# Kernel tuning notes

Measured on AMD Instinct MI355X. Metric: run time of the kernel, lower is better.

The kernel has to match this reference:

```python
import jax, jax.numpy as jnp
import numpy as np
import math

# dims
BSZ, L, D = 2, 4096, 1024
EXPAND, DS, NH, NG, DC, CS = 2, 128, 32, 1, 4, 64
DI = EXPAND * D            # 2048
HP = DI // NH              # 64 headdim
D_IN_PROJ = 2 * DI + 2 * NG * DS + NH  # 4384
CONV_DIM = DI + 2 * NG * DS            # 2304
EPS = 1e-5


def setup_inputs() -> dict:
    key = jax.random.key(0)
    ks = jax.random.split(key, 10)
    u = jax.random.normal(ks[0], (BSZ, L, D), dtype=jnp.float32)
    W_in = jax.random.normal(ks[1], (D, D_IN_PROJ), dtype=jnp.float32) / math.sqrt(D)
    conv_w = jax.random.normal(ks[2], (CONV_DIM, DC), dtype=jnp.float32) / math.sqrt(DC)
    conv_b = jnp.zeros((CONV_DIM,), dtype=jnp.float32)
    # dt init as in module: dt ~ logspace(1e-3, 0.1), dt_bias = inv softplus
    dt = jnp.exp(jax.random.uniform(ks[3], (NH,)) * (math.log(0.1) - math.log(0.001)) + math.log(0.001))
    dt = jnp.clip(dt, 1e-4, None)
    dt_bias = dt + jnp.log(-jnp.expm1(-dt))
    A_log = jnp.log(jax.random.uniform(ks[4], (NH,), minval=1.0, maxval=16.0))
    norm_w = jnp.ones((DI,), dtype=jnp.float32)
    norm_b = jnp.zeros((DI,), dtype=jnp.float32)
    W_out = jax.random.normal(ks[5], (DI, D), dtype=jnp.float32) / math.sqrt(DI)
    return {"u": u, "W_in": W_in, "conv_w": conv_w, "conv_b": conv_b,
            "dt_bias": dt_bias, "A_log": A_log, "norm_w": norm_w,
            "norm_b": norm_b, "W_out": W_out}


def _segsum(x):
    # x: (..., l) -> (..., l, l), out[i,j] = sum_{j<t<=i} x[t], -inf above diag
    cs = jnp.cumsum(x, axis=-1)
    d = cs[..., :, None] - cs[..., None, :]
    n = x.shape[-1]
    mask = jnp.tril(jnp.ones((n, n), dtype=bool))
    return jnp.where(mask, d, -jnp.inf)


def _ssd(x, A, Bm, Cm):
    # x: (b,l,h,p) already scaled by dt; A: (b,l,h) = a*dt; Bm,Cm: (b,l,h,n)
    b, l, h, p = x.shape
    nc = l // CS
    x = x.reshape(b, nc, CS, h, p)
    A = A.reshape(b, nc, CS, h).transpose(0, 3, 1, 2)          # (b,h,c,s)
    Bm = Bm.reshape(b, nc, CS, h, -1)
    Cm = Cm.reshape(b, nc, CS, h, -1)
    A_cum = jnp.cumsum(A, axis=-1)                              # (b,h,c,s)
    Lmat = jnp.exp(_segsum(A))                                  # (b,h,c,s,s)
    # intra-chunk (diagonal block) output
    Yd = jnp.einsum('bclhn,bcshn,bhcls,bcshp->bclhp', Cm, Bm, Lmat, x)
    # per-chunk final states
    decay_states = jnp.exp(A_cum[..., -1:] - A_cum)             # (b,h,c,s)
    states = jnp.einsum('bcshn,bhcs,bcshp->bchpn', Bm, decay_states, x)
    # inter-chunk recurrence (parallel via segsum over chunk decays)
    A_chunk = jnp.pad(A_cum[..., -1], ((0, 0), (0, 0), (1, 0)))  # (b,h,c+1)
    decay_chunk = jnp.exp(_segsum(A_chunk))                      # (b,h,c+1,c+1)
    states0 = jnp.concatenate([jnp.zeros_like(states[:, :1]), states], axis=1)
    new_states = jnp.einsum('bhzc,bchpn->bzhpn', decay_chunk, states0)
    states_in = new_states[:, :-1]                               # (b,c,h,p,n)
    state_decay = jnp.exp(A_cum)                                 # (b,h,c,s)
    Yoff = jnp.einsum('bcshn,bchpn,bhcs->bcshp', Cm, states_in, state_decay)
    return (Yd + Yoff).reshape(b, l, h, p)


def _causal_dwconv(x, w, b):
    # x: (B,L,C), depthwise causal conv, kernel w: (C,K), bias b: (C,)
    k = w.shape[1]
    xp = jnp.pad(x, ((0, 0), (k - 1, 0), (0, 0)))
    seqlen = x.shape[1]
    out = b
    for i in range(k):  # small fixed kernel loop (K=4)
        out = out + xp[:, i:i + seqlen, :] * w[:, i]
    return out


def reference(u, W_in, conv_w, conv_b, dt_bias, A_log, norm_w, norm_b, W_out):
    b, l, _ = u.shape
    zxbcdt = u @ W_in                                  # (b,l,2*DI+2*NG*DS+NH)
    z = zxbcdt[..., :DI]
    xBC = zxbcdt[..., DI:DI + CONV_DIM]
    dt = jax.nn.softplus(zxbcdt[..., -NH:] + dt_bias)  # (b,l,h)
    A = -jnp.exp(A_log)                                # (h,)
    xBC = jax.nn.silu(_causal_dwconv(xBC, conv_w, conv_b))
    x = xBC[..., :DI].reshape(b, l, NH, HP)
    Bv = xBC[..., DI:DI + NG * DS].reshape(b, l, NG, DS)
    Cv = xBC[..., DI + NG * DS:].reshape(b, l, NG, DS)
    # broadcast groups to heads
    rep = NH // NG
    Bh = jnp.repeat(Bv, rep, axis=2)                   # (b,l,h,n)
    Ch = jnp.repeat(Cv, rep, axis=2)
    y = _ssd(x * dt[..., None], A * dt, Bh, Ch)        # (b,l,h,p)
    y = y.reshape(b, l, DI)
    y = y * jax.nn.silu(z)                             # gated
    mu = jnp.mean(y, axis=-1, keepdims=True)
    var = jnp.mean(jnp.square(y - mu), axis=-1, keepdims=True)
    y = (y - mu) * jax.lax.rsqrt(var + EPS) * norm_w + norm_b
    return y @ W_out
```

## Files before the change

### kernel.cpp

```cpp
#include <hip/hip_runtime.h>
#include <hip/hip_bf16.h>
#include <math.h>


namespace {

constexpr int kB   = 2;
constexpr int kL   = 4096;
constexpr int kDI  = 2048;
constexpr int kDS  = 128;
constexpr int kNH  = 32;
constexpr int kHP  = 64;
constexpr int kDC  = 4;
constexpr int kCS  = 64;
constexpr int kNC  = kL / kCS;
constexpr int kDProj   = 2 * kDI + 2 * kDS + kNH;
constexpr int kDProjP  = 4480;
constexpr int kConvDim = kDI + 2 * kDS;
constexpr int kRows = kB * kL;
constexpr float kEps = 1e-5f;
constexpr int kTS = 136;
constexpr int kWS = 72;

typedef __bf16 bf16x8 __attribute__((ext_vector_type(8)));
typedef float f32x4 __attribute__((ext_vector_type(4)));
typedef unsigned short ushort8 __attribute__((ext_vector_type(8)));

__device__ inline float bu2f(unsigned short u) {
  union { unsigned int i; float f; } x; x.i = ((unsigned int)u) << 16; return x.f;
}
__device__ inline unsigned short f2bu(float f) {
  __hip_bfloat16 h = __float2bfloat16(f);
  return *reinterpret_cast<unsigned short*>(&h);
}

__device__ inline void store_out(float* C, size_t i, float v) { C[i] = v; }
__device__ inline void store_out(unsigned short* C, size_t i, float v) { C[i] = f2bu(v); }

__device__ inline void gld_lds16(const unsigned short* g, unsigned short* l) {
  __builtin_amdgcn_global_load_lds(
      (const __attribute__((address_space(1))) unsigned int*)g,
      (__attribute__((address_space(3))) unsigned int*)l, 16, 0, 0);
}

__global__ void cast_kernel(const float4* __restrict__ in, ushort4* __restrict__ out, int n4) {
  int i = blockIdx.x * 256 + threadIdx.x;
  if (i >= n4) return;
  float4 v = in[i];
  ushort4 o;
  o.x = f2bu(v.x); o.y = f2bu(v.y); o.z = f2bu(v.z); o.w = f2bu(v.w);
  out[i] = o;
}

__global__ void transpose_cast(const float* __restrict__ in, unsigned short* __restrict__ out,
                               int R, int C, const float* __restrict__ scale) {
  __shared__ float t[32][33];
  const int c0 = blockIdx.x * 32;
  const int r0 = blockIdx.y * 32;
  const int tx = threadIdx.x & 31, ty = threadIdx.x >> 5;
  for (int rr = ty; rr < 32; rr += 8) {
    int c = c0 + tx;
    float v = (c < C) ? in[(size_t)(r0 + rr) * C + c] : 0.f;
    if (scale) v *= scale[r0 + rr];
    t[rr][tx] = v;
  }
  __syncthreads();
  for (int cc = ty; cc < 32; cc += 8) {
    int orow = c0 + cc;
    out[(size_t)orow * R + r0 + tx] = f2bu(t[tx][cc]);
  }
}

__global__ void colsum_kernel(const float* __restrict__ W2, const float* __restrict__ wv,
                              const float* __restrict__ bv,
                              float* __restrict__ t1, float* __restrict__ t2) {
  __shared__ float p1[4][64], p2[4][64];
  const int nl = threadIdx.x & 63;
  const int ks = threadIdx.x >> 6;
  const int n = blockIdx.x * 64 + nl;
  float s1 = 0.f, s2 = 0.f;
  for (int k = ks * 512; k < ks * 512 + 512; k++) {
    float v = W2[(size_t)k * 1024 + n];
    s1 += wv[k] * v;
    s2 += bv[k] * v;
  }
  p1[ks][nl] = s1; p2[ks][nl] = s2;
  __syncthreads();
  if (threadIdx.x < 64) {
    t1[blockIdx.x * 64 + threadIdx.x] =
        p1[0][threadIdx.x] + p1[1][threadIdx.x] + p1[2][threadIdx.x] + p1[3][threadIdx.x];
    t2[blockIdx.x * 64 + threadIdx.x] =
        p2[0][threadIdx.x] + p2[1][threadIdx.x] + p2[2][threadIdx.x] + p2[3][threadIdx.x];
  }
}

template <typename OutT, bool FOLD>
__global__ __launch_bounds__(256, 3) void gemm_bt(const unsigned short* __restrict__ A,
                                                  const unsigned short* __restrict__ Bt,
                                                  OutT* __restrict__ C, int M, int N, int K,
                                                  const float* __restrict__ mu,
                                                  const float* __restrict__ rstd,
                                                  const float* __restrict__ t1,
                                                  const float* __restrict__ t2) {
  __shared__ __align__(16) unsigned short As[128 * 64];
  __shared__ __align__(16) unsigned short Bs[128 * 64];
  const int tid = threadIdx.x;
  const int wave = tid >> 6, lane = tid & 63;
  const int nwg = (int)(gridDim.x * gridDim.y);
  const int orig = (int)(blockIdx.y * gridDim.x + blockIdx.x);
  const int swz = (orig & 7) * (nwg >> 3) + (orig >> 3);
  const int bx = swz % (int)gridDim.x, by = swz / (int)gridDim.x;
  const int m0 = by * 128, n0 = bx * 128;
  const int wr = (wave >> 1) * 64, wc = (wave & 1) * 64;
  const int l8 = lane >> 3, s8 = lane & 7;
  const unsigned short* pA[4];
  const unsigned short* pB[4];
  unsigned short* lA[4];
  unsigned short* lB[4];
#pragma unroll
  for (int r = 0; r < 4; r++) {
    int q = wave * 4 + r;
    pA[r] = A + (size_t)(m0 + q * 8 + l8) * K + (s8 ^ l8) * 8;
    pB[r] = Bt + (size_t)(n0 + q * 8 + l8) * K + (s8 ^ l8) * 8;
    lA[r] = &As[q * 512];
    lB[r] = &Bs[q * 512];
  }
  const int fr = lane & 15;
  const int c4 = lane >> 4;
  const int sk0 = (c4 ^ (fr & 7)) * 8;
  const int sk1 = ((4 | c4) ^ (fr & 7)) * 8;
  f32x4 acc[4][4] = {};
  for (int k0 = 0; k0 < K; k0 += 64) {
#pragma unroll
    for (int r = 0; r < 4; r++) {
      gld_lds16(pA[r] + k0, lA[r]);
      gld_lds16(pB[r] + k0, lB[r]);
    }
    asm volatile("s_waitcnt vmcnt(0)" ::: "memory");
    __syncthreads();
    {
      bf16x8 af0[4], bf0[4];
#pragma unroll
      for (int i = 0; i < 4; i++) {
        af0[i] = *(const bf16x8*)&As[(wr + i * 16 + fr) * 64 + sk0];
        bf0[i] = *(const bf16x8*)&Bs[(wc + i * 16 + fr) * 64 + sk0];
      }
#pragma unroll
      for (int i = 0; i < 4; i++)
#pragma unroll
        for (int j = 0; j < 4; j++)
          acc[i][j] = __builtin_amdgcn_mfma_f32_16x16x32_bf16(af0[i], bf0[j], acc[i][j], 0, 0, 0);
    }
    {
      bf16x8 af1[4], bf1[4];
#pragma unroll
      for (int i = 0; i < 4; i++) {
        af1[i] = *(const bf16x8*)&As[(wr + i * 16 + fr) * 64 + sk1];
        bf1[i] = *(const bf16x8*)&Bs[(wc + i * 16 + fr) * 64 + sk1];
      }
#pragma unroll
      for (int i = 0; i < 4; i++)
#pragma unroll
        for (int j = 0; j < 4; j++)
          acc[i][j] = __builtin_amdgcn_mfma_f32_16x16x32_bf16(af1[i], bf1[j], acc[i][j], 0, 0, 0);
    }
    __syncthreads();
  }
  const int crow = (lane >> 4) * 4;
  const int ccol = lane & 15;
#pragma unroll
  for (int i = 0; i < 4; i++) {
#pragma unroll
    for (int j = 0; j < 4; j++) {
      int n = n0 + wc + j * 16 + ccol;
      if (n < N) {
        float c1 = FOLD ? t1[n] : 0.f;
        float c2 = FOLD ? t2[n] : 0.f;
#pragma unroll
        for (int r = 0; r < 4; r++) {
          int m = m0 + wr + i * 16 + crow + r;
          float v = acc[i][j][r];
          if (FOLD) v = rstd[m] * (v - mu[m] * c1) + c2;
          store_out(C, (size_t)m * N + n, v);
        }
      }
    }
  }
}

__global__ void dt_kernel(const unsigned short* __restrict__ zxbcdt,
                          const float* __restrict__ dt_bias,
                          float* __restrict__ dtbuf) {
  int idx = blockIdx.x * 256 + threadIdx.x;
  if (idx >= kRows * kNH) return;
  int row = idx >> 5, h = idx & 31;
  float x = bu2f(zxbcdt[(size_t)row * kDProj + (kDProj - kNH) + h]) + dt_bias[h];
  dtbuf[idx] = (x > 15.f) ? x : log1pf(expf(x));
}

__global__ void conv_silu_kernel(const unsigned short* __restrict__ zxbcdt,
                                 const float* __restrict__ conv_w,
                                 const float* __restrict__ conv_b,
                                 unsigned short* __restrict__ xbc_act) {
  int c4 = blockIdx.x * 256 + threadIdx.x;
  if (c4 >= kConvDim / 4) return;
  const int c = c4 * 4;
  const int r0 = blockIdx.y * 8;
  const int l0 = r0 & (kL - 1);
  float4 w[4];
  float bias[4];
#pragma unroll
  for (int q = 0; q < 4; q++) {
    w[q] = ((const float4*)conv_w)[c + q];
    bias[q] = conv_b[c + q];
  }
  float v[11][4];
#pragma unroll
  for (int i = 0; i < 11; i++) {
    int l = l0 - 3 + i;
    if (l >= 0) {
      ushort4 t = *(const ushort4*)&zxbcdt[(size_t)(r0 - 3 + i) * kDProj + kDI + c];
      v[i][0] = bu2f(t.x); v[i][1] = bu2f(t.y); v[i][2] = bu2f(t.z); v[i][3] = bu2f(t.w);
    } else {
      v[i][0] = v[i][1] = v[i][2] = v[i][3] = 0.f;
    }
  }
#pragma unroll
  for (int j = 0; j < 8; j++) {
    ushort4 o;
    unsigned short* op = (unsigned short*)&o;
#pragma unroll
    for (int q = 0; q < 4; q++) {
      float a = bias[q] + v[j][q] * w[q].x + v[j + 1][q] * w[q].y +
                v[j + 2][q] * w[q].z + v[j + 3][q] * w[q].w;
      op[q] = f2bu(a / (1.f + expf(-a)));
    }
    *(ushort4*)&xbc_act[(size_t)(r0 + j) * kConvDim + c] = o;
  }
}

__global__ __launch_bounds__(256) void chunk_state_kernel(
    const unsigned short* __restrict__ xbc_act,
    const float* __restrict__ dtbuf,
    const float* __restrict__ A_log,
    unsigned short* __restrict__ states,
    float* __restrict__ asum) {
  const int id = blockIdx.x;
  const int h = id & 31;
  const int c = (id >> 5) & (kNC - 1);
  const int b = id >> 11;
  const int tid = threadIdx.x;
  const int wave = tid >> 6, lane = tid & 63;
  __shared__ __align__(16) unsigned short sBT[kDS * kWS];
  __shared__ __align__(16) unsigned short sxd[kCS * kWS];
  __shared__ float s_dt[kCS];
  __shared__ float s_acum[kCS];
  const int l0 = b * kL + c * kCS;
  if (tid < kCS) s_dt[tid] = dtbuf[(size_t)(l0 + tid) * kNH + h];
  __syncthreads();
  if (tid == 0) {
    float A = -expf(A_log[h]);
    float run = 0.f;
    for (int s = 0; s < kCS; s++) { run += A * s_dt[s]; s_acum[s] = run; }
    asum[id] = run;
  }
  __syncthreads();
  const float total = s_acum[kCS - 1];
  for (int e = tid; e < kCS * kDS; e += 256) {
    int s = e >> 7, n = e & 127;
    sBT[n * kWS + s] = xbc_act[(size_t)(l0 + s) * kConvDim + kDI + n];
  }
  for (int e = tid; e < kCS * kHP; e += 256) {
    int s = e >> 6, p = e & 63;
    float xv = bu2f(xbc_act[(size_t)(l0 + s) * kConvDim + h * kHP + p]);
    sxd[p * kWS + s] = f2bu(xv * s_dt[s] * expf(total - s_acum[s]));
  }
  __syncthreads();
  const int arow = wave * 16 + (lane & 15);
  const int fk = (lane >> 4) * 8;
  f32x4 acc[8] = {};
#pragma unroll
  for (int kk = 0; kk < 2; kk++) {
    bf16x8 a = *(const bf16x8*)&sxd[arow * kWS + kk * 32 + fk];
#pragma unroll
    for (int j = 0; j < 8; j++) {
      bf16x8 bb = *(const bf16x8*)&sBT[(j * 16 + (lane & 15)) * kWS + kk * 32 + fk];
      acc[j] = __builtin_amdgcn_mfma_f32_16x16x32_bf16(a, bb, acc[j], 0, 0, 0);
    }
  }
  const int prow = wave * 16 + (lane >> 4) * 4;
  const int ncol = lane & 15;
  size_t base = (size_t)id * (kHP * kDS);
#pragma unroll
  for (int j = 0; j < 8; j++)
#pragma unroll
    for (int r = 0; r < 4; r++)
      states[base + (size_t)(prow + r) * kDS + j * 16 + ncol] = f2bu(acc[j][r]);
}

__global__ void scan_kernel(unsigned short* __restrict__ states,
                            const float* __restrict__ asum) {
  const int blk = blockIdx.x;
  const int seg = blk & 7;
  const int bh = blk >> 3;
  const int h = bh & 31, b = bh >> 5;
  const int e4 = seg * 256 + threadIdx.x;
  const size_t cstride = (size_t)kNH * 2048;
  ushort4* p = (ushort4*)states + ((size_t)(b * kNC) * kNH + h) * 2048 + e4;
  const float* ap = asum + (b * kNC) * kNH + h;
  float c0 = 0.f, c1 = 0.f, c2 = 0.f, c3 = 0.f;
  ushort4 t = p[0];
  float dec = expf(ap[0]);
  for (int c = 0; c < kNC; c++) {
    ushort4 tn = t;
    float decn = dec;
    if (c + 1 < kNC) {
      tn = p[(size_t)(c + 1) * cstride];
      decn = expf(ap[(c + 1) * kNH]);
    }
    ushort4 o;
    o.x = f2bu(c0); o.y = f2bu(c1); o.z = f2bu(c2); o.w = f2bu(c3);
    p[(size_t)c * cstride] = o;
    c0 = c0 * dec + bu2f(t.x);
    c1 = c1 * dec + bu2f(t.y);
    c2 = c2 * dec + bu2f(t.z);
    c3 = c3 * dec + bu2f(t.w);
    t = tn; dec = decn;
  }
}

__global__ __launch_bounds__(256) void y_kernel(
    const unsigned short* __restrict__ xbc_act,
    const unsigned short* __restrict__ zxbcdt,
    const unsigned short* __restrict__ states_in,
    const float* __restrict__ dtbuf,
    const float* __restrict__ A_log,
    unsigned short* __restrict__ ybuf,
    float* __restrict__ pS, float* __restrict__ pQ) {
  const int id = blockIdx.x;
  const int hg = id & 7;
  const int c = (id >> 3) & (kNC - 1);
  const int b = id >> 9;
  const int tid = threadIdx.x;
  const int wave = tid >> 6, lane = tid & 63;
  __shared__ __align__(16) unsigned short sC[kCS * kTS];
  __shared__ __align__(16) unsigned short sB[kCS * kTS];
  __shared__ __align__(16) unsigned short sxd[kCS * kWS];
  __shared__ __align__(16) unsigned short sW[kCS * kWS];
  __shared__ float s_dt[4][kCS];
  __shared__ float s_acum[4][kCS];
  const int l0 = b * kL + c * kCS;
  {
    int hh = tid >> 6, s = tid & 63;
    s_dt[hh][s] = dtbuf[(size_t)(l0 + s) * kNH + hg * 4 + hh];
  }
  __syncthreads();
  if (tid < 4) {
    float A = -expf(A_log[hg * 4 + tid]);
    float run = 0.f;
    for (int s = 0; s < kCS; s++) { run += A * s_dt[tid][s]; s_acum[tid][s] = run; }
  }
  for (int e = tid; e < kCS * 16; e += 256) {
    int row = e >> 4, c8 = (e & 15) * 8;
    size_t rb = (size_t)(l0 + row) * kConvDim;
    *(ushort8*)&sB[row * kTS + c8] = *(const ushort8*)&xbc_act[rb + kDI + c8];
    *(ushort8*)&sC[row * kTS + c8] = *(const ushort8*)&xbc_act[rb + kDI + kDS + c8];
  }
  __syncthreads();
  const int arow = wave * 16 + (lane & 15);
  const int fk = (lane >> 4) * 8;
  f32x4 accG[4] = {};
#pragma unroll
  for (int kk = 0; kk < 4; kk++) {
    bf16x8 a = *(const bf16x8*)&sC[arow * kTS + kk * 32 + fk];
#pragma unroll
    for (int j = 0; j < 4; j++) {
      bf16x8 bb = *(const bf16x8*)&sB[(j * 16 + (lane & 15)) * kTS + kk * 32 + fk];
      accG[j] = __builtin_amdgcn_mfma_f32_16x16x32_bf16(a, bb, accG[j], 0, 0, 0);
    }
  }
  const int lrow = wave * 16 + (lane >> 4) * 4;
  const size_t sbase = (size_t)((b * kNC + c) * kNH) * (kHP * kDS);
  float rS[4] = {}, rQ[4] = {};
  for (int hh = 0; hh < 4; hh++) {
    const int h = hg * 4 + hh;
    __syncthreads();
    for (int e = tid; e < kCS * kHP; e += 256) {
      int s = e >> 6, p = e & 63;
      float xv = bu2f(xbc_act[(size_t)(l0 + s) * kConvDim + h * kHP + p]);
      sxd[p * kWS + s] = f2bu(xv * s_dt[hh][s]);
    }
#pragma unroll
    for (int j = 0; j < 4; j++) {
      int scol = j * 16 + (lane & 15);
      float as = s_acum[hh][scol];
#pragma unroll
      for (int r = 0; r < 4; r++) {
        int l = lrow + r;
        float w = (scol <= l) ? accG[j][r] * expf(s_acum[hh][l] - as) : 0.f;
        sW[l * kWS + scol] = f2bu(w);
      }
    }
    for (int e = tid; e < kCS * 16; e += 256) {
      int row = e >> 4, c8 = (e & 15) * 8;
      *(ushort8*)&sB[row * kTS + c8] =
          *(const ushort8*)&states_in[sbase + (size_t)h * (kHP * kDS) + row * kDS + c8];
    }
    __syncthreads();
    f32x4 accY[4] = {};
#pragma unroll
    for (int kk = 0; kk < 2; kk++) {
      bf16x8 a = *(const bf16x8*)&sW[arow * kWS + kk * 32 + fk];
#pragma unroll
      for (int j = 0; j < 4; j++) {
        bf16x8 bb = *(const bf16x8*)&sxd[(j * 16 + (lane & 15)) * kWS + kk * 32 + fk];
        accY[j] = __builtin_amdgcn_mfma_f32_16x16x32_bf16(a, bb, accY[j], 0, 0, 0);
      }
    }
    f32x4 accO[4] = {};
#pragma unroll
    for (int kk = 0; kk < 4; kk++) {
      bf16x8 a = *(const bf16x8*)&sC[arow * kTS + kk * 32 + fk];
#pragma unroll
      for (int j = 0; j < 4; j++) {
        bf16x8 bb = *(const bf16x8*)&sB[(j * 16 + (lane & 15)) * kTS + kk * 32 + fk];
        accO[j] = __builtin_amdgcn_mfma_f32_16x16x32_bf16(a, bb, accO[j], 0, 0, 0);
      }
    }
#pragma unroll
    for (int r = 0; r < 4; r++) {
      int l = lrow + r;
      float el = expf(s_acum[hh][l]);
      size_t zrow = (size_t)(l0 + l) * kDProj + h * kHP;
      size_t yrow = (size_t)(l0 + l) * kDI + h * kHP;
#pragma unroll
      for (int j = 0; j < 4; j++) {
        int p = j * 16 + (lane & 15);
        float yv = accY[j][r] + el * accO[j][r];
        float z = bu2f(zxbcdt[zrow + p]);
        yv *= z / (1.f + expf(-z));
        rS[r] += yv;
        rQ[r] += yv * yv;
        ybuf[yrow + p] = f2bu(yv);
      }
    }
  }
#pragma unroll
  for (int m = 1; m < 16; m <<= 1) {
#pragma unroll
    for (int r = 0; r < 4; r++) {
      rS[r] += __shfl_xor(rS[r], m);
      rQ[r] += __shfl_xor(rQ[r], m);
    }
  }
  if ((lane & 15) == 0) {
#pragma unroll
    for (int r = 0; r < 4; r++) {
      int row = l0 + lrow + r;
      pS[(size_t)row * 8 + hg] = rS[r];
      pQ[(size_t)row * 8 + hg] = rQ[r];
    }
  }
}

__global__ void ln_reduce(const float* __restrict__ pS, const float* __restrict__ pQ,
                          float* __restrict__ mu, float* __restrict__ rstd) {
  int row = blockIdx.x * 256 + threadIdx.x;
  if (row >= kRows) return;
  float s = 0.f, q = 0.f;
#pragma unroll
  for (int i = 0; i < 8; i++) { s += pS[(size_t)row * 8 + i]; q += pQ[(size_t)row * 8 + i]; }
  float m = s / kDI;
  mu[row] = m;
  rstd[row] = rsqrtf(q / kDI - m * m + kEps);
}

}

extern "C" void kernel_launch(void* const* d_in, const int* in_sizes, int n_in,
                              void* d_out, int out_size, void* d_ws, size_t ws_size,
                              hipStream_t stream) {
  const float* u       = (const float*)d_in[0];
  const float* W_in    = (const float*)d_in[1];
  const float* conv_w  = (const float*)d_in[2];
  const float* conv_b  = (const float*)d_in[3];
  const float* dt_bias = (const float*)d_in[4];
  const float* A_log   = (const float*)d_in[5];
  const float* norm_w  = (const float*)d_in[6];
  const float* norm_b  = (const float*)d_in[7];
  const float* W_out   = (const float*)d_in[8];
  float* out = (float*)d_out;

  char* ws = (char*)d_ws;
  size_t off = 0;
  auto alloc = [&](size_t bytes) {
    void* p = ws + off;
    off += (bytes + 255) & ~(size_t)255;
    return p;
  };
  unsigned short* zxbcdt = (unsigned short*)alloc((size_t)kRows * kDProj * 2);
  unsigned short* xbc    = (unsigned short*)alloc((size_t)kRows * kConvDim * 2);
  float* dtb             = (float*)alloc((size_t)kRows * kNH * 4);
  float* asum            = (float*)alloc((size_t)kB * kNC * kNH * 4);
  unsigned short* A1     = (unsigned short*)alloc((size_t)kRows * 1024 * 2);
  unsigned short* Bt1    = (unsigned short*)alloc((size_t)kDProjP * 1024 * 2);
  unsigned short* states = (unsigned short*)alloc((size_t)kB * kNC * kNH * kHP * kDS * 2);
  unsigned short* Bt2    = (unsigned short*)alloc((size_t)1024 * kDI * 2);
  unsigned short* ybuf   = (unsigned short*)alloc((size_t)kRows * kDI * 2);
  float* mu              = (float*)alloc((size_t)kRows * 4);
  float* rstd            = (float*)alloc((size_t)kRows * 4);
  float* t1              = (float*)alloc(1024 * 4);
  float* t2              = (float*)alloc(1024 * 4);
  float* pS              = (float*)alloc((size_t)kRows * 8 * 4);
  float* pQ              = (float*)alloc((size_t)kRows * 8 * 4);
  (void)ws_size; (void)in_sizes; (void)n_in; (void)out_size;

  cast_kernel<<<(kRows * 1024 / 4 + 255) / 256, 256, 0, stream>>>(
      (const float4*)u, (ushort4*)A1, kRows * 1024 / 4);
  transpose_cast<<<dim3(kDProjP / 32, 1024 / 32), 256, 0, stream>>>(
      W_in, Bt1, 1024, kDProj, nullptr);
  transpose_cast<<<dim3(1024 / 32, 2048 / 32), 256, 0, stream>>>(
      W_out, Bt2, 2048, 1024, norm_w);
  colsum_kernel<<<16, 256, 0, stream>>>(W_out, norm_w, norm_b, t1, t2);
  gemm_bt<unsigned short, false><<<dim3(kDProjP / 128, kRows / 128), 256, 0, stream>>>(
      A1, Bt1, zxbcdt, kRows, kDProj, 1024, nullptr, nullptr, nullptr, nullptr);
  dt_kernel<<<(kRows * kNH + 255) / 256, 256, 0, stream>>>(zxbcdt, dt_bias, dtb);
  conv_silu_kernel<<<dim3(3, kRows / 8), 256, 0, stream>>>(zxbcdt, conv_w, conv_b, xbc);
  chunk_state_kernel<<<kB * kNC * kNH, 256, 0, stream>>>(xbc, dtb, A_log, states, asum);
  scan_kernel<<<kB * kNH * 8, 256, 0, stream>>>(states, asum);
  y_kernel<<<kB * kNC * 8, 256, 0, stream>>>(xbc, zxbcdt, states, dtb, A_log, ybuf, pS, pQ);
  ln_reduce<<<kRows / 256, 256, 0, stream>>>(pS, pQ, mu, rstd);
  gemm_bt<float, true><<<dim3(1024 / 128, kRows / 128), 256, 0, stream>>>(
      ybuf, Bt2, out, kRows, 1024, 2048, mu, rstd, t1, t2);
}
```

Before: 437.6 us.

## Fuse dt softplus into GEMM epilogue, parallelize cumsums, widen scan grid

Computes the softplus of dt directly in the in-projection GEMM epilogue and removes the separate dt_kernel launch and its re-read of zxbcdt. The serial per-chunk cumulative sums of A*dt in chunk_state and y_kernel become wave-level shuffle prefix scans. The inter-chunk scan now uses ushort2 elements with twice as many blocks and prefetches two chunks ahead. conv_silu blocks are resized to 192 threads so 3 blocks exactly cover the 576 channel groups. The GEMM epilogue gains a branch and transcendental math on its last columns. The dt values are now computed from the fp32 accumulator rather than the bf16-rounded output, which changes numerics slightly.

```diff
diff --git a/kernel.cpp b/kernel.cpp
--- a/kernel.cpp
+++ b/kernel.cpp
@@ -101,7 +101,9 @@
                                                   const float* __restrict__ mu,
                                                   const float* __restrict__ rstd,
                                                   const float* __restrict__ t1,
-                                                  const float* __restrict__ t2) {
+                                                  const float* __restrict__ t2,
+                                                  const float* __restrict__ dt_bias,
+                                                  float* __restrict__ dtb) {
   __shared__ __align__(16) unsigned short As[128 * 64];
   __shared__ __align__(16) unsigned short Bs[128 * 64];
   const int tid = threadIdx.x;
@@ -182,27 +184,22 @@
           float v = acc[i][j][r];
           if (FOLD) v = rstd[m] * (v - mu[m] * c1) + c2;
           store_out(C, (size_t)m * N + n, v);
+          if (!FOLD && n >= kDProj - kNH) {
+            int hh = n - (kDProj - kNH);
+            float x = v + dt_bias[hh];
+            dtb[(size_t)m * kNH + hh] = (x > 15.f) ? x : log1pf(expf(x));
+          }
         }
       }
     }
   }
-}
-
-__global__ void dt_kernel(const unsigned short* __restrict__ zxbcdt,
-                          const float* __restrict__ dt_bias,
-                          float* __restrict__ dtbuf) {
-  int idx = blockIdx.x * 256 + threadIdx.x;
-  if (idx >= kRows * kNH) return;
-  int row = idx >> 5, h = idx & 31;
-  float x = bu2f(zxbcdt[(size_t)row * kDProj + (kDProj - kNH) + h]) + dt_bias[h];
-  dtbuf[idx] = (x > 15.f) ? x : log1pf(expf(x));
 }
 
 __global__ void conv_silu_kernel(const unsigned short* __restrict__ zxbcdt,
                                  const float* __restrict__ conv_w,
                                  const float* __restrict__ conv_b,
                                  unsigned short* __restrict__ xbc_act) {
-  int c4 = blockIdx.x * 256 + threadIdx.x;
+  int c4 = blockIdx.x * 192 + threadIdx.x;
   if (c4 >= kConvDim / 4) return;
   const int c = c4 * 4;
   const int r0 = blockIdx.y * 8;
@@ -258,11 +255,16 @@
   const int l0 = b * kL + c * kCS;
   if (tid < kCS) s_dt[tid] = dtbuf[(size_t)(l0 + tid) * kNH + h];
   __syncthreads();
-  if (tid == 0) {
+  if (tid < 64) {
     float A = -expf(A_log[h]);
-    float run = 0.f;
-    for (int s = 0; s < kCS; s++) { run += A * s_dt[s]; s_acum[s] = run; }
-    asum[id] = run;
+    float v = A * s_dt[tid];
+#pragma unroll
+    for (int off = 1; off < 64; off <<= 1) {
+      float u = __shfl_up(v, off);
+      if (tid >= off) v += u;
+    }
+    s_acum[tid] = v;
+    if (tid == 63) asum[id] = v;
   }
   __syncthreads();
   const float total = s_acum[kCS - 1];
@@ -301,31 +303,32 @@
 __global__ void scan_kernel(unsigned short* __restrict__ states,
                             const float* __restrict__ asum) {
   const int blk = blockIdx.x;
-  const int seg = blk & 7;
-  const int bh = blk >> 3;
+  const int seg = blk & 15;
+  const int bh = blk >> 4;
   const int h = bh & 31, b = bh >> 5;
-  const int e4 = seg * 256 + threadIdx.x;
-  const size_t cstride = (size_t)kNH * 2048;
-  ushort4* p = (ushort4*)states + ((size_t)(b * kNC) * kNH + h) * 2048 + e4;
+  const int e2 = seg * 256 + threadIdx.x;
+  const size_t cstride = (size_t)kNH * 4096;
+  ushort2* p = (ushort2*)states + ((size_t)(b * kNC) * kNH + h) * 4096 + e2;
   const float* ap = asum + (b * kNC) * kNH + h;
-  float c0 = 0.f, c1 = 0.f, c2 = 0.f, c3 = 0.f;
-  ushort4 t = p[0];
+  float c0 = 0.f, c1 = 0.f;
+  ushort2 t = p[0];
   float dec = expf(ap[0]);
+  ushort2 t1v = p[cstride];
+  float dec1 = expf(ap[kNH]);
   for (int c = 0; c < kNC; c++) {
-    ushort4 tn = t;
-    float decn = dec;
-    if (c + 1 < kNC) {
-      tn = p[(size_t)(c + 1) * cstride];
-      decn = expf(ap[(c + 1) * kNH]);
-    }
-    ushort4 o;
-    o.x = f2bu(c0); o.y = f2bu(c1); o.z = f2bu(c2); o.w = f2bu(c3);
+    ushort2 t2v = t1v;
+    float dec2 = dec1;
+    if (c + 2 < kNC) {
+      t2v = p[(size_t)(c + 2) * cstride];
+      dec2 = expf(ap[(c + 2) * kNH]);
+    }
+    ushort2 o;
+    o.x = f2bu(c0); o.y = f2bu(c1);
     p[(size_t)c * cstride] = o;
     c0 = c0 * dec + bu2f(t.x);
     c1 = c1 * dec + bu2f(t.y);
-    c2 = c2 * dec + bu2f(t.z);
-    c3 = c3 * dec + bu2f(t.w);
-    t = tn; dec = decn;
+    t = t1v; dec = dec1;
+    t1v = t2v; dec1 = dec2;
   }
 }
 
@@ -355,10 +358,16 @@
     s_dt[hh][s] = dtbuf[(size_t)(l0 + s) * kNH + hg * 4 + hh];
   }
   __syncthreads();
-  if (tid < 4) {
-    float A = -expf(A_log[hg * 4 + tid]);
-    float run = 0.f;
-    for (int s = 0; s < kCS; s++) { run += A * s_dt[tid][s]; s_acum[tid][s] = run; }
+  {
+    int hh = tid >> 6, s = tid & 63;
+    float A = -expf(A_log[hg * 4 + hh]);
+    float v = A * s_dt[hh][s];
+#pragma unroll
+    for (int off = 1; off < 64; off <<= 1) {
+      float u = __shfl_up(v, off);
+      if (s >= off) v += u;
+    }
+    s_acum[hh][s] = v;
   }
   for (int e = tid; e < kCS * 16; e += 256) {
     int row = e >> 4, c8 = (e & 15) * 8;
@@ -523,13 +532,13 @@
       W_out, Bt2, 2048, 1024, norm_w);
   colsum_kernel<<<16, 256, 0, stream>>>(W_out, norm_w, norm_b, t1, t2);
   gemm_bt<unsigned short, false><<<dim3(kDProjP / 128, kRows / 128), 256, 0, stream>>>(
-      A1, Bt1, zxbcdt, kRows, kDProj, 1024, nullptr, nullptr, nullptr, nullptr);
-  dt_kernel<<<(kRows * kNH + 255) / 256, 256, 0, stream>>>(zxbcdt, dt_bias, dtb);
-  conv_silu_kernel<<<dim3(3, kRows / 8), 256, 0, stream>>>(zxbcdt, conv_w, conv_b, xbc);
+      A1, Bt1, zxbcdt, kRows, kDProj, 1024, nullptr, nullptr, nullptr, nullptr,
+      dt_bias, dtb);
+  conv_silu_kernel<<<dim3(3, kRows / 8), 192, 0, stream>>>(zxbcdt, conv_w, conv_b, xbc);
   chunk_state_kernel<<<kB * kNC * kNH, 256, 0, stream>>>(xbc, dtb, A_log, states, asum);
-  scan_kernel<<<kB * kNH * 8, 256, 0, stream>>>(states, asum);
+  scan_kernel<<<kB * kNH * 16, 256, 0, stream>>>(states, asum);
   y_kernel<<<kB * kNC * 8, 256, 0, stream>>>(xbc, zxbcdt, states, dtb, A_log, ybuf, pS, pQ);
   ln_reduce<<<kRows / 256, 256, 0, stream>>>(pS, pQ, mu, rstd);
   gemm_bt<float, true><<<dim3(1024 / 128, kRows / 128), 256, 0, stream>>>(
-      ybuf, Bt2, out, kRows, 1024, 2048, mu, rstd, t1, t2);
-}
+      ybuf, Bt2, out, kRows, 1024, 2048, mu, rstd, t1, t2, nullptr, nullptr);
+}
```

Result: no change. 441.3 us (+0.8%).
